# Performance work log

Measured on AMD Instinct MI355X. Metric: run time of the kernel, lower is better.

The kernel has to match this reference:

```python
import jax, jax.numpy as jnp
import numpy as np

B, N, K, A = 2, 4096, 20, 12
DIMS = [32, 64, 128, 256, 512]
POOL_RATE, POOL_K = 4, 4


def knn_index(v, k):
    # v: (b, n, 3) -> (b, n, k) nearest neighbors, self excluded
    d2 = jnp.sum(v * v, axis=-1)
    dist = d2[:, :, None] + d2[:, None, :] - 2.0 * jnp.einsum('bnd,bmd->bnm', v, v)
    _, idx = jax.lax.top_k(-dist, k + 1)
    return idx[:, :, 1:]


def gather_pos(v, idx):
    return jax.vmap(lambda vv, ii: vv[ii])(v, idx)  # (b, n, k, 3)


def gather_fea(fm, idx):
    return jax.vmap(lambda f, ii: f[:, ii, :])(fm, idx)  # (b, c, n, k, a)


def nbr_dirs(v, idx):
    d = gather_pos(v, idx) - v[:, :, None, :]
    return d / (jnp.linalg.norm(d, axis=-1, keepdims=True) + 1e-8)


def conv_surface(idx, v, K0):
    # K0: (C0, A, 3) learned direction kernels; output (b, C0, n, A)
    d = nbr_dirs(v, idx)  # (b,n,k,3)
    theta = jax.nn.relu(jnp.einsum('bnkd,cad->bnkca', d, K0))
    return jnp.transpose(jnp.max(theta, axis=2), (0, 2, 1, 3))


def equi_conv(idx, v, fm, dirs, Wc, bc, Ws):
    # fm: (b, cin, n, a) -> (b, cout, n, a)
    d = nbr_dirs(v, idx)
    theta = jax.nn.relu(jnp.einsum('bnkd,ad->bnka', d, dirs))  # (b,n,k,a)
    fn = gather_fea(fm, idx)  # (b,cin,n,k,a)
    fs = jnp.einsum('bcnka,co->bonka', fn, Ws) * theta[:, None]
    fs = jnp.max(fs, axis=3)  # max over neighbors -> (b,cout,n,a)
    fc = jnp.einsum('bcna,co->bona', fm, Wc) + bc[None, :, None, None]
    return fc + fs


def batchnorm(x, g, b):
    m = jnp.mean(x, axis=(0, 2, 3), keepdims=True)
    var = jnp.var(x, axis=(0, 2, 3), keepdims=True)
    return (x - m) * jax.lax.rsqrt(var + 1e-5) * g[None, :, None, None] + b[None, :, None, None]


def pool(v, fm):
    idx = knn_index(v, POOL_K)
    fn = jnp.max(gather_fea(fm, idx), axis=3)
    fm_p = jnp.maximum(fm, fn)
    sel = jnp.arange(0, v.shape[1], POOL_RATE)  # strided subsample
    return v[:, sel], fm_p[:, :, sel]


def fea_of(fm):
    return jnp.transpose(jnp.max(fm, axis=-1), (0, 2, 1))  # (b,n,c)


def setup_inputs() -> dict:
    key = jax.random.key(0)
    ks = iter(jax.random.split(key, 32))
    p = {'vertices': jax.random.normal(next(ks), (B, N, 3), jnp.float32)}
    p['K0'] = jax.random.normal(next(ks), (DIMS[0], A, 3), jnp.float32) * 0.1
    for i, (ci, co) in enumerate(zip(DIMS[:4], DIMS[1:]), start=1):
        s = 1.0 / np.sqrt(ci).astype(np.float32)
        p[f'dirs{i}'] = jax.random.normal(next(ks), (A, 3), jnp.float32) * 0.1
        p[f'Wc{i}'] = jax.random.normal(next(ks), (ci, co), jnp.float32) * s
        p[f'bc{i}'] = jnp.zeros((co,), jnp.float32)
        p[f'Ws{i}'] = jax.random.normal(next(ks), (ci, co), jnp.float32) * s
    for i, c in enumerate([DIMS[1], DIMS[2], DIMS[3]], start=1):
        p[f'g{i}'] = jnp.ones((c,), jnp.float32)
        p[f'b{i}'] = jnp.zeros((c,), jnp.float32)
    return p


def reference(vertices, K0, dirs1, Wc1, bc1, Ws1, dirs2, Wc2, bc2, Ws2,
              dirs3, Wc3, bc3, Ws3, dirs4, Wc4, bc4, Ws4,
              g1, b1, g2, b2, g3, b3):
    idx = knn_index(vertices, K)
    fm0 = jax.nn.relu(conv_surface(idx, vertices, K0))
    fm1 = jax.nn.relu(batchnorm(equi_conv(idx, vertices, fm0, dirs1, Wc1, bc1, Ws1), g1, b1))
    v1, fmp1 = pool(vertices, fm1)
    idx1 = knn_index(v1, min(K, v1.shape[1] // 8))
    fm2 = jax.nn.relu(batchnorm(equi_conv(idx1, v1, fmp1, dirs2, Wc2, bc2, Ws2), g2, b2))
    fm3 = jax.nn.relu(batchnorm(equi_conv(idx1, v1, fm2, dirs3, Wc3, bc3, Ws3), g3, b3))
    v2, fmp2 = pool(v1, fm3)
    idx2 = knn_index(v2, min(K, v2.shape[1] // 8))
    fm4 = equi_conv(idx2, v2, fmp2, dirs4, Wc4, bc4, Ws4)
    return fea_of(fm0), fea_of(fm1), fea_of(fm2), fea_of(fm3), fea_of(fm4)
```

## Files before the change

### kernel.cpp

```cpp
#include <hip/hip_runtime.h>
#include <hip/hip_bf16.h>
#include <math.h>

typedef unsigned short u16;
typedef unsigned long long u64;
#define DEV static __device__ __forceinline__

constexpr int Bz = 2, N0 = 4096, N1 = 1024, N2 = 256, KNN = 20, NA = 12;
constexpr int C0 = 32, C1 = 64, C2 = 128, C3 = 256, C4 = 512;
constexpr int BNG = 32;

constexpr size_t OFF_V0F   = 0;
constexpr size_t OFF_V1F   = 32768;
constexpr size_t OFF_V2F   = 40960;
constexpr size_t OFF_K0F   = 43008;
constexpr size_t OFF_DIRS  = 44160;
constexpr size_t OFF_WC    = 44304;
constexpr size_t OFF_WS    = 218384;
constexpr size_t OFF_BC    = 392464;
constexpr size_t OFF_BN    = 393424;
constexpr size_t OFF_FLAG  = 394832;
constexpr size_t OFF_IDX0  = 394848;
constexpr size_t OFF_IDX1  = 558688;
constexpr size_t OFF_IDX2  = 599648;
constexpr size_t OFF_PART  = 609888;
constexpr size_t PART_SZ   = 28672;
constexpr size_t OFF_HALF  = OFF_PART + PART_SZ;

constexpr size_t HA = 0;
constexpr size_t HB = 3145728;
constexpr size_t HG = 9437184;
constexpr size_t HP = HG + 3145728;

constexpr size_t OUT0 = 0;
constexpr size_t OUT1 = OUT0 + (size_t)Bz*N0*C0;
constexpr size_t OUT2 = OUT1 + (size_t)Bz*N0*C1;
constexpr size_t OUT3 = OUT2 + (size_t)Bz*N1*C2;
constexpr size_t OUT4 = OUT3 + (size_t)Bz*N1*C3;

DEV float b2f(u16 v) { return __uint_as_float(((unsigned int)v) << 16); }
DEV u16 f2b(float f) {
  unsigned int u = __float_as_uint(f);
  unsigned int lsb = (u >> 16) & 1u;
  return (u16)((u + 0x7fffu + lsb) >> 16);
}
DEV unsigned packb(float a, float b) {
  return (unsigned)f2b(a) | ((unsigned)f2b(b) << 16);
}

DEV u64 shflx64(u64 v, int m) {
  int lo = __shfl_xor((int)(unsigned)v, m, 64);
  int hi = __shfl_xor((int)(unsigned)(v >> 32), m, 64);
  return ((u64)(unsigned)hi << 32) | (unsigned)lo;
}
DEV int mbcnt64(u64 m) {
  return __builtin_amdgcn_mbcnt_hi((unsigned)(m >> 32),
         __builtin_amdgcn_mbcnt_lo((unsigned)m, 0));
}

DEV void st12(float* dst, const float* v) {
  float4 a{v[0],v[1],v[2],v[3]}, b{v[4],v[5],v[6],v[7]}, c{v[8],v[9],v[10],v[11]};
  ((float4*)dst)[0] = a; ((float4*)dst)[1] = b; ((float4*)dst)[2] = c;
}
DEV void st12(u16* dst, const float* v) {
  uint2 a{packb(v[0],v[1]), packb(v[2],v[3])};
  uint2 b{packb(v[4],v[5]), packb(v[6],v[7])};
  uint2 c{packb(v[8],v[9]), packb(v[10],v[11])};
  ((uint2*)dst)[0] = a; ((uint2*)dst)[1] = b; ((uint2*)dst)[2] = c;
}

struct InPtrs { const void* p[24]; };

__global__ void eq_convert_all(InPtrs in, float* ws) {
  __shared__ int sflag;
  {
    const u16* v = (const u16*)in.p[0];
    if (threadIdx.x < 64) {
      int bad = 0;
      #pragma unroll
      for (int j = 0; j < 4; ++j) {
        unsigned u = v[threadIdx.x*4 + j];
        int ex = (u >> 7) & 0xFF;
        bad += (((u & 0x7FFFu) != 0u) && (ex < 64 || ex > 191)) ? 1 : 0;
      }
      int tot = bad;
      #pragma unroll
      for (int s = 32; s > 0; s >>= 1) tot += __shfl_xor(tot, s, 64);
      if (threadIdx.x == 0) sflag = (tot >= 8) ? 1 : 0;
    }
    __syncthreads();
  }
  int f32mode = sflag;
  int t = blockIdx.x * blockDim.x + threadIdx.x;
  if (t < Bz*N0) {
    float x, y, z;
    if (f32mode) { const float* v = (const float*)in.p[0]; x=v[t*3]; y=v[t*3+1]; z=v[t*3+2]; }
    else { const u16* v = (const u16*)in.p[0]; x=b2f(v[t*3]); y=b2f(v[t*3+1]); z=b2f(v[t*3+2]); }
    float4 o; o.x=x; o.y=y; o.z=z; o.w=(x*x + y*y) + z*z;
    ((float4*)(ws + OFF_V0F))[t] = o;
    int b = t / N0, i = t % N0;
    if ((i & 3) == 0)  ((float4*)(ws + OFF_V1F))[b*N1 + (i >> 2)] = o;
    if ((i & 15) == 0) ((float4*)(ws + OFF_V2F))[b*N2 + (i >> 4)] = o;
    return;
  }
  int r = t - Bz*N0;
  if (r >= 351312) {
    int z = r - 351312;
    if (z < (int)PART_SZ) ws[OFF_PART + z] = 0.f;
    return;
  }
  const int cnt[23] = {1152, 36,2048,64,2048, 36,8192,128,8192,
                       36,32768,256,32768, 36,131072,512,131072,
                       64,64,128,128,256,256};
  const size_t off[23] = {OFF_K0F,
    OFF_DIRS+0,   OFF_WC+0,     OFF_BC+0,   OFF_WS+0,
    OFF_DIRS+36,  OFF_WC+2048,  OFF_BC+64,  OFF_WS+2048,
    OFF_DIRS+72,  OFF_WC+10240, OFF_BC+192, OFF_WS+10240,
    OFF_DIRS+108, OFF_WC+43008, OFF_BC+448, OFF_WS+43008,
    OFF_BN+0, OFF_BN+64, OFF_BN+128, OFF_BN+256, OFF_BN+384, OFF_BN+640};
  for (int i = 0; i < 23; ++i) {
    if (r < cnt[i]) {
      float val = f32mode ? ((const float*)in.p[i+1])[r] : b2f(((const u16*)in.p[i+1])[r]);
      ws[off[i] + r] = val;
      return;
    }
    r -= cnt[i];
  }
}

template<int NPTS>
DEV void knn_body(int blk, const float4* __restrict__ vf, int* __restrict__ idx_out,
                  char* smem) {
  constexpr int CPL = NPTS/64;
  constexpr int TILE = (NPTS < 512) ? NPTS : 512;
  constexpr int NT = NPTS / TILE;
  float4* tile = (float4*)smem;
  u64* selw_base = (u64*)(smem + TILE*16);
  int* extr_base = (int*)(smem + TILE*16 + 4*64*8);
  int wave = threadIdx.x >> 6, lane = threadIdx.x & 63;
  int tid = threadIdx.x;
  u64* selw = selw_base + wave*64;
  int* extrw = extr_base + wave*24;
  int qid = blk*4 + wave;
  int b = qid / NPTS, q = qid % NPTS;
  const float4* vb = vf + (size_t)b*NPTS;
  float4 vq = vb[q];
  const unsigned DINF = 0xFFFFFFFFu;
  unsigned d1=DINF, d2=DINF, d3=DINF, d4=DINF;
  int i1=0x3FFFFFFF, i2=0x3FFFFFFF, i3=0x3FFFFFFF, i4=0x3FFFFFFF;
  for (int tt = 0; tt < NT; ++tt) {
    __syncthreads();
    for (int i = tid; i < TILE; i += 256) tile[i] = vb[tt*TILE + i];
    __syncthreads();
    #pragma unroll 4
    for (int j = 0; j < TILE/64; ++j) {
      int cl = j*64 + lane;
      float4 vc = tile[cl];
      int c = tt*TILE + cl;
      float dt = (vq.x*vc.x + vq.y*vc.y) + vq.z*vc.z;
      float d = (vq.w + vc.w) - 2.0f*dt;
      unsigned u = __float_as_uint(d);
      unsigned ud = u ^ ((unsigned)(((int)u) >> 31) | 0x80000000u);
      bool lt1 = ud < d1, lt2 = ud < d2, lt3 = ud < d3, lt4 = ud < d4;
      d4 = lt3 ? d3 : (lt4 ? ud : d4);  i4 = lt3 ? i3 : (lt4 ? c : i4);
      d3 = lt2 ? d2 : (lt3 ? ud : d3);  i3 = lt2 ? i2 : (lt3 ? c : i3);
      d2 = lt1 ? d1 : (lt2 ? ud : d2);  i2 = lt1 ? i1 : (lt2 ? c : i2);
      d1 = lt1 ? ud : d1;               i1 = lt1 ? c  : i1;
    }
  }
  unsigned p = 0;
  for (int bit = 31; bit >= 0; --bit) {
    unsigned T = p | (1u << bit);
    u64 m1 = __ballot(d1 < T), m2 = __ballot(d2 < T);
    u64 m3 = __ballot(d3 < T), m4 = __ballot(d4 < T);
    int cnt = __popcll(m1) + __popcll(m2) + __popcll(m3) + __popcll(m4);
    if (cnt < KNN+1) p = T;
  }
  size_t obase = (size_t)qid*KNN;
  bool need_fb = false;
  if (CPL > 4) {
    need_fb = (__ballot(d4 <= p) != 0ULL);
  }
  if (!need_fb) {
    bool p1 = d1 <= p, p2 = d2 <= p, p3 = d3 <= p, p4 = d4 <= p;
    u64 m1 = __ballot(p1), m2 = __ballot(p2), m3 = __ballot(p3), m4 = __ballot(p4);
    int c1 = __popcll(m1), c2 = __popcll(m2), c3 = __popcll(m3), c4 = __popcll(m4);
    int S = c1 + c2 + c3 + c4;
    if (S > 63) need_fb = true;
    else {
      if (p1) selw[mbcnt64(m1)] = ((u64)d1 << 32) | (unsigned)i1;
      if (p2) selw[c1 + mbcnt64(m2)] = ((u64)d2 << 32) | (unsigned)i2;
      if (p3) selw[c1 + c2 + mbcnt64(m3)] = ((u64)d3 << 32) | (unsigned)i3;
      if (p4) selw[c1 + c2 + c3 + mbcnt64(m4)] = ((u64)d4 << 32) | (unsigned)i4;
      if (lane < S) {
        u64 mykey = selw[lane];
        int rank = 0;
        for (int j = 0; j < S; ++j) rank += (selw[j] < mykey) ? 1 : 0;
        if (rank >= 1 && rank <= KNN)
          idx_out[obase + rank - 1] = (int)(unsigned)(mykey & 0xFFFFFFFFu);
      }
    }
  }
  if (need_fb) {
    const u64 KINF = ~0ULL;
    u64 k1 = ((u64)d1 << 32) | (unsigned)i1;
    u64 k2 = ((u64)d2 << 32) | (unsigned)i2;
    u64 k3 = ((u64)d3 << 32) | (unsigned)i3;
    u64 k4 = ((u64)d4 << 32) | (unsigned)i4;
    for (int r = 0; r < KNN+1; ++r) {
      u64 g = k1;
      #pragma unroll
      for (int s = 32; s; s >>= 1) { u64 o = shflx64(g, s); g = (o < g) ? o : g; }
      int gidx = (int)(g & 0xFFFFFFFFu);
      if (lane == 0) {
        extrw[r] = gidx;
        if (r > 0) idx_out[obase + r - 1] = gidx;
      }
      if (r < KNN && lane == (gidx & 63)) {
        k1 = k2; k2 = k3; k3 = k4; k4 = KINF;
        if (k1 == KINF) {
          for (int j = 0; j < CPL; ++j) {
            int c = j*64 + lane;
            float4 vc = vb[c];
            float dt = (vq.x*vc.x + vq.y*vc.y) + vq.z*vc.z;
            float d = (vq.w + vc.w) - 2.0f*dt;
            unsigned u = __float_as_uint(d);
            unsigned ud = u ^ ((unsigned)(((int)u) >> 31) | 0x80000000u);
            u64 k = ((u64)ud << 32) | (unsigned)c;
            bool ex = false;
            for (int e = 0; e <= r; ++e) ex |= (extrw[e] == c);
            if (!ex) {
              bool lt1 = k < k1, lt2 = k < k2, lt3 = k < k3, lt4 = k < k4;
              k4 = lt3 ? k3 : (lt4 ? k : k4);
              k3 = lt2 ? k2 : (lt3 ? k : k3);
              k2 = lt1 ? k1 : (lt2 ? k : k2);
              k1 = lt1 ? k  : k1;
            }
          }
        }
      }
    }
  }
}

__global__ __launch_bounds__(256) void eq_knn_all(
    const float4* __restrict__ v0, int* __restrict__ i0,
    const float4* __restrict__ v1, int* __restrict__ i1,
    const float4* __restrict__ v2, int* __restrict__ i2) {
  __shared__ __align__(16) char smem[512*16 + 4*64*8 + 4*24*4];
  int blk = blockIdx.x;
  constexpr int NB0 = Bz*N0/4, NB1 = Bz*N1/4;
  if (blk < NB0)            knn_body<N0>(blk, v0, i0, smem);
  else if (blk < NB0+NB1)   knn_body<N1>(blk - NB0, v1, i1, smem);
  else                      knn_body<N2>(blk - NB0 - NB1, v2, i2, smem);
}

__global__ __launch_bounds__(128) void eq_conv_surface(
    const float4* __restrict__ v0f, const int* __restrict__ idx0,
    const float* __restrict__ K0f, u16* __restrict__ fm0, float* __restrict__ out0) {
  int bq = blockIdx.x;
  int b = bq >> 12;
  __shared__ float dk[KNN][3];
  __shared__ float row[C0*NA];
  int tid = threadIdx.x;
  if (tid < KNN) {
    int m = idx0[(size_t)bq*KNN + tid];
    float4 vq = v0f[bq];
    float4 vm = v0f[(size_t)b*N0 + m];
    float dx = vm.x - vq.x, dy = vm.y - vq.y, dz = vm.z - vq.z;
    float nrm = sqrtf((dx*dx + dy*dy) + dz*dz) + 1e-8f;
    dk[tid][0] = dx/nrm; dk[tid][1] = dy/nrm; dk[tid][2] = dz/nrm;
  }
  __syncthreads();
  for (int t4 = tid; t4 < C0*NA/4; t4 += 128) {
    const float* kd = K0f + (size_t)t4*12;
    float4 k0 = *(const float4*)(kd);
    float4 k1 = *(const float4*)(kd + 4);
    float4 k2 = *(const float4*)(kd + 8);
    float m0=0.f, m1=0.f, m2=0.f, m3=0.f;
    #pragma unroll
    for (int k = 0; k < KNN; ++k) {
      float dx = dk[k][0], dy = dk[k][1], dz = dk[k][2];
      m0 = fmaxf(m0, (dx*k0.x + dy*k0.y) + dz*k0.z);
      m1 = fmaxf(m1, (dx*k0.w + dy*k1.x) + dz*k1.y);
      m2 = fmaxf(m2, (dx*k1.z + dy*k1.w) + dz*k2.x);
      m3 = fmaxf(m3, (dx*k2.y + dy*k2.z) + dz*k2.w);
    }
    uint2 r; r.x = packb(m0, m1); r.y = packb(m2, m3);
    ((uint2*)fm0)[(size_t)bq*(C0*NA/4) + t4] = r;
    row[4*t4+0] = m0; row[4*t4+1] = m1; row[4*t4+2] = m2; row[4*t4+3] = m3;
  }
  __syncthreads();
  if (tid < C0) {
    float m = row[tid*NA];
    #pragma unroll
    for (int a = 1; a < NA; ++a) m = fmaxf(m, row[tid*NA + a]);
    out0[(size_t)bq*C0 + tid] = m;
  }
}

template<int CI, int CO, typename TO>
__global__ __launch_bounds__(256) void eq_linear4(
    const u16* __restrict__ in, const float* __restrict__ Wc,
    const float* __restrict__ Ws, const float* __restrict__ bias,
    TO* __restrict__ fc, u16* __restrict__ g) {
  constexpr int PPB = 512 / CO;
  constexpr int RS = CI*NA + 4;
  __shared__ float lds[PPB*RS];
  int tid = threadIdx.x;
  int mat = blockIdx.x & 1;
  int pt0 = (blockIdx.x >> 1) * PPB;
  constexpr int E = PPB*CI*NA;
  for (int t = tid; t < E; t += 256) {
    int pt = t / (CI*NA), r = t % (CI*NA);
    lds[pt*RS + r] = b2f(in[((size_t)(pt0+pt))*CI*NA + r]);
  }
  __syncthreads();
  constexpr int TPP = CO/2;
  int opair = tid % TPP, pt = tid / TPP;
  int o0 = opair*2;
  const float* W = mat ? Ws : Wc;
  const float* row = lds + pt*RS;
  float a0[NA], a1[NA];
  #pragma unroll
  for (int a = 0; a < NA; ++a) { a0[a]=0.f; a1[a]=0.f; }
  #pragma unroll 4
  for (int c = 0; c < CI; ++c) {
    float2 w2 = *(const float2*)(W + (size_t)c*CO + o0);
    float4 i0 = *(const float4*)(row + c*NA);
    float4 i1 = *(const float4*)(row + c*NA + 4);
    float4 i2 = *(const float4*)(row + c*NA + 8);
    float iv[NA] = {i0.x,i0.y,i0.z,i0.w, i1.x,i1.y,i1.z,i1.w, i2.x,i2.y,i2.z,i2.w};
    #pragma unroll
    for (int a = 0; a < NA; ++a) {
      a0[a] += iv[a]*w2.x; a1[a] += iv[a]*w2.y;
    }
  }
  size_t ptg = pt0 + pt;
  if (mat == 0) {
    float b0 = bias[o0], b1 = bias[o0+1];
    #pragma unroll
    for (int a = 0; a < NA; ++a) { a0[a] += b0; a1[a] += b1; }
    st12(fc + ((size_t)ptg*CO + o0)*NA, a0);
    st12(fc + ((size_t)ptg*CO + o0 + 1)*NA, a1);
  } else {
    st12(g + ((size_t)ptg*CO + o0)*NA, a0);
    st12(g + ((size_t)ptg*CO + o0 + 1)*NA, a1);
  }
}

__global__ __launch_bounds__(256) void eq_fsmax(
    const u16* __restrict__ g, const float4* __restrict__ vf,
    const float* __restrict__ dirs, const int* __restrict__ idx,
    u16* __restrict__ out, float* __restrict__ part, int npts, int co) {
  int bq = blockIdx.x;
  int b = bq / npts;
  __shared__ float th[KNN*NA];
  __shared__ float dk[KNN][3];
  __shared__ int nb[KNN];
  __shared__ float sstat[2][C3];
  int tid = threadIdx.x;
  if (tid < KNN) {
    int m = idx[(size_t)bq*KNN + tid];
    nb[tid] = m;
    float4 vq = vf[bq];
    float4 vm = vf[(size_t)b*npts + m];
    float dx = vm.x - vq.x, dy = vm.y - vq.y, dz = vm.z - vq.z;
    float nrm = sqrtf((dx*dx + dy*dy) + dz*dz) + 1e-8f;
    dk[tid][0] = dx/nrm; dk[tid][1] = dy/nrm; dk[tid][2] = dz/nrm;
  }
  sstat[0][tid] = 0.f; sstat[1][tid] = 0.f;
  __syncthreads();
  if (tid < KNN*NA) {
    int k = tid / NA, a = tid % NA;
    float s = (dk[k][0]*dirs[a*3] + dk[k][1]*dirs[a*3+1]) + dk[k][2]*dirs[a*3+2];
    th[tid] = fmaxf(s, 0.f);
  }
  __syncthreads();
  int quarter = co*NA/4;
  uint2* dst = (uint2*)(out + (size_t)bq*co*NA);
  const uint2* gb = (const uint2*)(g + (size_t)b*npts*co*NA);
  for (int t4 = tid; t4 < quarter; t4 += 256) {
    int a = (4*t4) % NA;
    const float* tha = th + a;
    float m0=-3.0e38f, m1=-3.0e38f, m2=-3.0e38f, m3=-3.0e38f;
    #pragma unroll 5
    for (int k = 0; k < KNN; ++k) {
      uint2 pv = gb[(size_t)nb[k]*quarter + t4];
      float4 tv = *(const float4*)(tha + k*NA);
      m0 = fmaxf(m0, tv.x*b2f((u16)(pv.x)));
      m1 = fmaxf(m1, tv.y*b2f((u16)(pv.x >> 16)));
      m2 = fmaxf(m2, tv.z*b2f((u16)(pv.y)));
      m3 = fmaxf(m3, tv.w*b2f((u16)(pv.y >> 16)));
    }
    uint2 d = dst[t4];
    float v0 = b2f((u16)d.x) + m0;
    float v1 = b2f((u16)(d.x >> 16)) + m1;
    float v2 = b2f((u16)d.y) + m2;
    float v3 = b2f((u16)(d.y >> 16)) + m3;
    uint2 r; r.x = packb(v0, v1); r.y = packb(v2, v3);
    dst[t4] = r;
    int ch = t4 / 3;
    atomicAdd(&sstat[0][ch], (v0 + v1) + (v2 + v3));
    atomicAdd(&sstat[1][ch], (v0*v0 + v1*v1) + (v2*v2 + v3*v3));
  }
  __syncthreads();
  if (tid < co) {
    float* pg = part + (size_t)(bq & (BNG-1))*2*co;
    atomicAdd(&pg[tid], sstat[0][tid]);
    atomicAdd(&pg[co + tid], sstat[1][tid]);
  }
}

template<int SPL>
__global__ __launch_bounds__(256) void eq_fsmax_fea(
    const u16* __restrict__ g, const float* __restrict__ fcin,
    const float4* __restrict__ vf, const float* __restrict__ dirs,
    const int* __restrict__ idx, float* __restrict__ outfea,
    int npts, int co) {
  constexpr int CHUNK = C4 / SPL;
  int part = blockIdx.x % SPL;
  int bq = blockIdx.x / SPL;
  int b = bq / npts;
  __shared__ float th[KNN*NA];
  __shared__ float dk[KNN][3];
  __shared__ int nb[KNN];
  __shared__ float row[CHUNK*NA];
  int tid = threadIdx.x;
  if (tid < KNN) {
    int m = idx[(size_t)bq*KNN + tid];
    nb[tid] = m;
    float4 vq = vf[bq];
    float4 vm = vf[(size_t)b*npts + m];
    float dx = vm.x - vq.x, dy = vm.y - vq.y, dz = vm.z - vq.z;
    float nrm = sqrtf((dx*dx + dy*dy) + dz*dz) + 1e-8f;
    dk[tid][0] = dx/nrm; dk[tid][1] = dy/nrm; dk[tid][2] = dz/nrm;
  }
  __syncthreads();
  if (tid < KNN*NA) {
    int k = tid / NA, a = tid % NA;
    float s = (dk[k][0]*dirs[a*3] + dk[k][1]*dirs[a*3+1]) + dk[k][2]*dirs[a*3+2];
    th[tid] = fmaxf(s, 0.f);
  }
  __syncthreads();
  int o0 = part * CHUNK;
  const float4* fcr = (const float4*)(fcin + ((size_t)bq*co + o0)*NA);
  const uint2* gb = (const uint2*)(g + (size_t)b*npts*co*NA + (size_t)o0*NA);
  int gquarter = co*NA/4;
  for (int t4 = tid; t4 < CHUNK*NA/4; t4 += 256) {
    int a = (4*t4) % NA;
    const float* tha = th + a;
    float m0=-3.0e38f, m1=-3.0e38f, m2=-3.0e38f, m3=-3.0e38f;
    #pragma unroll 5
    for (int k = 0; k < KNN; ++k) {
      uint2 pv = gb[(size_t)nb[k]*gquarter + t4];
      float4 tv = *(const float4*)(tha + k*NA);
      m0 = fmaxf(m0, tv.x*b2f((u16)(pv.x)));
      m1 = fmaxf(m1, tv.y*b2f((u16)(pv.x >> 16)));
      m2 = fmaxf(m2, tv.z*b2f((u16)(pv.y)));
      m3 = fmaxf(m3, tv.w*b2f((u16)(pv.y >> 16)));
    }
    float4 fc4 = fcr[t4];
    row[4*t4+0] = fc4.x + m0;
    row[4*t4+1] = fc4.y + m1;
    row[4*t4+2] = fc4.z + m2;
    row[4*t4+3] = fc4.w + m3;
  }
  __syncthreads();
  for (int o = tid; o < CHUNK; o += 256) {
    float m = row[o*NA];
    #pragma unroll
    for (int a = 1; a < NA; ++a) m = fmaxf(m, row[o*NA + a]);
    outfea[(size_t)bq*co + o0 + o] = m;
  }
}

__global__ __launch_bounds__(256) void eq_bnrelu_fea(
    u16* __restrict__ fm, const float* __restrict__ part,
    const float* __restrict__ gamma, const float* __restrict__ beta,
    float* __restrict__ outfea, int npts, int co) {
  int bq = blockIdx.x;
  int tid = threadIdx.x;
  __shared__ float sc[C3], sh[C3];
  __shared__ float row[C3*NA];
  for (int o = tid; o < co; o += 256) {
    float s = 0.f, s2 = 0.f;
    for (int g = 0; g < BNG; ++g) {
      s  += part[(size_t)g*2*co + o];
      s2 += part[(size_t)g*2*co + co + o];
    }
    float cnt = (float)(Bz*npts*NA);
    float mean = s / cnt;
    float var = fmaxf(s2 / cnt - mean*mean, 0.f);
    float inv = 1.0f / sqrtf(var + 1e-5f);
    sc[o] = gamma[o] * inv;
    sh[o] = beta[o] - mean * gamma[o] * inv;
  }
  __syncthreads();
  uint2* p = (uint2*)(fm + (size_t)bq*co*NA);
  int quarter = co*NA/4;
  for (int t4 = tid; t4 < quarter; t4 += 256) {
    int o = (4*t4) / NA;
    float s = sc[o], h = sh[o];
    uint2 pv = p[t4];
    float v0 = fmaxf(b2f((u16)pv.x)*s + h, 0.f);
    float v1 = fmaxf(b2f((u16)(pv.x >> 16))*s + h, 0.f);
    float v2 = fmaxf(b2f((u16)pv.y)*s + h, 0.f);
    float v3 = fmaxf(b2f((u16)(pv.y >> 16))*s + h, 0.f);
    uint2 r; r.x = packb(v0, v1); r.y = packb(v2, v3);
    p[t4] = r;
    row[4*t4+0] = v0; row[4*t4+1] = v1; row[4*t4+2] = v2; row[4*t4+3] = v3;
  }
  __syncthreads();
  for (int o = tid; o < co; o += 256) {
    float m = row[o*NA];
    #pragma unroll
    for (int a = 1; a < NA; ++a) m = fmaxf(m, row[o*NA + a]);
    outfea[(size_t)bq*co + o] = m;
  }
}

__global__ __launch_bounds__(256) void eq_pool(
    const u16* __restrict__ fm, const int* __restrict__ idx,
    u16* __restrict__ fmp, int npts, int c) {
  int ns = npts / 4;
  int bj = blockIdx.x;
  int b = bj / ns, j = bj % ns;
  int q = 4*j;
  size_t bq = (size_t)b*npts + q;
  __shared__ int nb[4];
  if (threadIdx.x < 4) nb[threadIdx.x] = idx[bq*KNN + threadIdx.x];
  __syncthreads();
  int quarter = c*NA/4;
  const uint2* base = (const uint2*)(fm + (size_t)b*npts*c*NA);
  const uint2* p0 = base + (size_t)q*quarter;
  uint2* dst = (uint2*)(fmp + (size_t)bj*c*NA);
  for (int t4 = threadIdx.x; t4 < quarter; t4 += 256) {
    uint2 v = p0[t4];
    float m0 = b2f((u16)v.x), m1 = b2f((u16)(v.x >> 16));
    float m2 = b2f((u16)v.y), m3 = b2f((u16)(v.y >> 16));
    #pragma unroll
    for (int kk = 0; kk < 4; ++kk) {
      uint2 w = base[(size_t)nb[kk]*quarter + t4];
      m0 = fmaxf(m0, b2f((u16)w.x));
      m1 = fmaxf(m1, b2f((u16)(w.x >> 16)));
      m2 = fmaxf(m2, b2f((u16)w.y));
      m3 = fmaxf(m3, b2f((u16)(w.y >> 16)));
    }
    uint2 r; r.x = packb(m0, m1); r.y = packb(m2, m3);
    dst[t4] = r;
  }
}

extern "C" void kernel_launch(void* const* d_in, const int* in_sizes, int n_in,
                              void* d_out, int out_size, void* d_ws, size_t ws_size,
                              hipStream_t stream) {
  float* ws = (float*)d_ws;
  float* out = (float*)d_out;
  u16* arena = (u16*)(ws + OFF_HALF);

  InPtrs ip;
  for (int i = 0; i < 24; ++i) ip.p[i] = d_in[i];

  float4* v0f = (float4*)(ws + OFF_V0F);
  float4* v1f = (float4*)(ws + OFF_V1F);
  float4* v2f = (float4*)(ws + OFF_V2F);
  int* idx0 = (int*)(ws + OFF_IDX0);
  int* idx1 = (int*)(ws + OFF_IDX1);
  int* idx2 = (int*)(ws + OFF_IDX2);
  u16* bufA = arena + HA;
  u16* bufB = arena + HB;
  float* fc4f = (float*)(arena + HB);
  u16* bufG = arena + HG;
  u16* bufP = arena + HP;
  float* partA = ws + OFF_PART;
  float* partB = ws + OFF_PART + 4096;
  float* partC = ws + OFF_PART + 12288;
  const float* DIRS = ws + OFF_DIRS;

  {
    int total = Bz*N0 + 351312 + (int)PART_SZ;
    eq_convert_all<<<(total + 255)/256, 256, 0, stream>>>(ip, ws);
  }

  eq_knn_all<<<Bz*N0/4 + Bz*N1/4 + Bz*N2/4, 256, 0, stream>>>(v0f, idx0, v1f, idx1, v2f, idx2);
  eq_conv_surface<<<Bz*N0, 128, 0, stream>>>(v0f, idx0, ws + OFF_K0F, bufA, out + OUT0);

  eq_linear4<C0, C1, u16><<<(Bz*N0/8)*2, 256, 0, stream>>>(bufA, ws + OFF_WC + 0, ws + OFF_WS + 0,
                                                           ws + OFF_BC + 0, bufB, bufG);
  eq_fsmax<<<Bz*N0, 256, 0, stream>>>(bufG, v0f, DIRS + 0, idx0, bufB, partA, N0, C1);
  eq_bnrelu_fea<<<Bz*N0, 256, 0, stream>>>(bufB, partA, ws + OFF_BN + 0, ws + OFF_BN + 64,
                                           out + OUT1, N0, C1);

  eq_pool<<<Bz*N1, 256, 0, stream>>>(bufB, idx0, bufP, N0, C1);

  eq_linear4<C1, C2, u16><<<(Bz*N1/4)*2, 256, 0, stream>>>(bufP, ws + OFF_WC + 2048, ws + OFF_WS + 2048,
                                                           ws + OFF_BC + 64, bufA, bufG);
  eq_fsmax<<<Bz*N1, 256, 0, stream>>>(bufG, v1f, DIRS + 36, idx1, bufA, partB, N1, C2);
  eq_bnrelu_fea<<<Bz*N1, 256, 0, stream>>>(bufA, partB, ws + OFF_BN + 128, ws + OFF_BN + 256,
                                           out + OUT2, N1, C2);

  eq_linear4<C2, C3, u16><<<(Bz*N1/2)*2, 256, 0, stream>>>(bufA, ws + OFF_WC + 10240, ws + OFF_WS + 10240,
                                                           ws + OFF_BC + 192, bufB, bufG);
  eq_fsmax<<<Bz*N1, 256, 0, stream>>>(bufG, v1f, DIRS + 72, idx1, bufB, partC, N1, C3);
  eq_bnrelu_fea<<<Bz*N1, 256, 0, stream>>>(bufB, partC, ws + OFF_BN + 384, ws + OFF_BN + 640,
                                           out + OUT3, N1, C3);

  eq_pool<<<Bz*N2, 256, 0, stream>>>(bufB, idx1, bufP, N1, C3);

  eq_linear4<C3, C4, float><<<(Bz*N2)*2, 256, 0, stream>>>(bufP, ws + OFF_WC + 43008, ws + OFF_WS + 43008,
                                                           ws + OFF_BC + 448, fc4f, bufG);
  eq_fsmax_fea<4><<<Bz*N2*4, 256, 0, stream>>>(bufG, fc4f, v2f, DIRS + 108, idx2, out + OUT4, N2, C4);
}
```

Before: 493.8 us.

## Track distance-only top-4 in kNN and recover indices with second threshold pass

The per-lane top-4 insertion now keeps only the distance keys and uses min/max networks, with no index registers or index selects. After the ballot-based threshold search, a second pass over the candidates recomputes distances and compacts those under the threshold into shared memory along with their indices. Tiles grow to 1024 points and the next tile is register-prefetched to overlap global loads with compute. The cost is recomputing every distance once more and a larger shared-memory footprint per block, which may reduce occupancy.

```diff
diff --git a/kernel.cpp b/kernel.cpp
--- a/kernel.cpp
+++ b/kernel.cpp
@@ -128,12 +128,23 @@
   }
 }
 
+DEV unsigned umin(unsigned a, unsigned b) { return a < b ? a : b; }
+DEV unsigned umax(unsigned a, unsigned b) { return a > b ? a : b; }
+
+DEV unsigned cand_ud(const float4 vq, const float4 vc) {
+  float dt = fmaf(vq.x, vc.x, fmaf(vq.y, vc.y, vq.z*vc.z));
+  float d  = fmaf(-2.0f, dt, vq.w + vc.w);
+  unsigned u = __float_as_uint(d);
+  return u ^ ((unsigned)(((int)u) >> 31) | 0x80000000u);
+}
+
 template<int NPTS>
 DEV void knn_body(int blk, const float4* __restrict__ vf, int* __restrict__ idx_out,
                   char* smem) {
   constexpr int CPL = NPTS/64;
-  constexpr int TILE = (NPTS < 512) ? NPTS : 512;
+  constexpr int TILE = (NPTS < 1024) ? NPTS : 1024;
   constexpr int NT = NPTS / TILE;
+  constexpr int LPT = TILE/256;
   float4* tile = (float4*)smem;
   u64* selw_base = (u64*)(smem + TILE*16);
   int* extr_base = (int*)(smem + TILE*16 + 4*64*8);
@@ -145,96 +156,125 @@
   int b = qid / NPTS, q = qid % NPTS;
   const float4* vb = vf + (size_t)b*NPTS;
   float4 vq = vb[q];
-  const unsigned DINF = 0xFFFFFFFFu;
-  unsigned d1=DINF, d2=DINF, d3=DINF, d4=DINF;
-  int i1=0x3FFFFFFF, i2=0x3FFFFFFF, i3=0x3FFFFFFF, i4=0x3FFFFFFF;
+
+  float4 pf[LPT];
+  #pragma unroll
+  for (int i = 0; i < LPT; ++i) pf[i] = vb[tid + i*256];
+  #pragma unroll
+  for (int i = 0; i < LPT; ++i) tile[tid + i*256] = pf[i];
+  __syncthreads();
+
+  unsigned k1=~0u, k2=~0u, k3=~0u, k4=~0u;
   for (int tt = 0; tt < NT; ++tt) {
-    __syncthreads();
-    for (int i = tid; i < TILE; i += 256) tile[i] = vb[tt*TILE + i];
-    __syncthreads();
+    if (tt+1 < NT) {
+      #pragma unroll
+      for (int i = 0; i < LPT; ++i) pf[i] = vb[(tt+1)*TILE + tid + i*256];
+    } else if (NT > 1) {
+      #pragma unroll
+      for (int i = 0; i < LPT; ++i) pf[i] = vb[tid + i*256];
+    }
     #pragma unroll 4
     for (int j = 0; j < TILE/64; ++j) {
-      int cl = j*64 + lane;
-      float4 vc = tile[cl];
-      int c = tt*TILE + cl;
-      float dt = (vq.x*vc.x + vq.y*vc.y) + vq.z*vc.z;
-      float d = (vq.w + vc.w) - 2.0f*dt;
-      unsigned u = __float_as_uint(d);
-      unsigned ud = u ^ ((unsigned)(((int)u) >> 31) | 0x80000000u);
-      bool lt1 = ud < d1, lt2 = ud < d2, lt3 = ud < d3, lt4 = ud < d4;
-      d4 = lt3 ? d3 : (lt4 ? ud : d4);  i4 = lt3 ? i3 : (lt4 ? c : i4);
-      d3 = lt2 ? d2 : (lt3 ? ud : d3);  i3 = lt2 ? i2 : (lt3 ? c : i3);
-      d2 = lt1 ? d1 : (lt2 ? ud : d2);  i2 = lt1 ? i1 : (lt2 ? c : i2);
-      d1 = lt1 ? ud : d1;               i1 = lt1 ? c  : i1;
-    }
-  }
+      float4 vc = tile[j*64 + lane];
+      unsigned key = cand_ud(vq, vc);
+      unsigned nk1 = umin(key, k1);
+      unsigned nk2 = umin(umax(key, k1), k2);
+      unsigned nk3 = umin(umax(key, k2), k3);
+      unsigned nk4 = umin(umax(key, k3), k4);
+      k1 = nk1; k2 = nk2; k3 = nk3; k4 = nk4;
+    }
+    if (tt+1 < NT || NT > 1) {
+      __syncthreads();
+      #pragma unroll
+      for (int i = 0; i < LPT; ++i) tile[tid + i*256] = pf[i];
+      __syncthreads();
+    }
+  }
+
   unsigned p = 0;
   for (int bit = 31; bit >= 0; --bit) {
     unsigned T = p | (1u << bit);
-    u64 m1 = __ballot(d1 < T), m2 = __ballot(d2 < T);
-    u64 m3 = __ballot(d3 < T), m4 = __ballot(d4 < T);
+    u64 m1 = __ballot(k1 < T), m2 = __ballot(k2 < T);
+    u64 m3 = __ballot(k3 < T), m4 = __ballot(k4 < T);
     int cnt = __popcll(m1) + __popcll(m2) + __popcll(m3) + __popcll(m4);
     if (cnt < KNN+1) p = T;
   }
   size_t obase = (size_t)qid*KNN;
-  bool need_fb = false;
-  if (CPL > 4) {
-    need_fb = (__ballot(d4 <= p) != 0ULL);
-  }
+  bool need_fb = (CPL > 4) && (__ballot(k4 <= p) != 0ULL);
+
+  int base = 0;
+  for (int tt = 0; tt < NT; ++tt) {
+    if (tt+1 < NT) {
+      #pragma unroll
+      for (int i = 0; i < LPT; ++i) pf[i] = vb[(tt+1)*TILE + tid + i*256];
+    }
+    if (!need_fb) {
+      #pragma unroll 4
+      for (int j = 0; j < TILE/64; ++j) {
+        float4 vc = tile[j*64 + lane];
+        unsigned ud = cand_ud(vq, vc);
+        bool sel = (ud <= p);
+        u64 m = __ballot(sel);
+        int pos = base + mbcnt64(m);
+        if (sel && pos < 64) {
+          int c = tt*TILE + j*64 + lane;
+          selw[pos] = ((u64)ud << 32) | (unsigned)c;
+        }
+        base += __popcll(m);
+      }
+    }
+    if (tt+1 < NT) {
+      __syncthreads();
+      #pragma unroll
+      for (int i = 0; i < LPT; ++i) tile[tid + i*256] = pf[i];
+      __syncthreads();
+    }
+  }
+
   if (!need_fb) {
-    bool p1 = d1 <= p, p2 = d2 <= p, p3 = d3 <= p, p4 = d4 <= p;
-    u64 m1 = __ballot(p1), m2 = __ballot(p2), m3 = __ballot(p3), m4 = __ballot(p4);
-    int c1 = __popcll(m1), c2 = __popcll(m2), c3 = __popcll(m3), c4 = __popcll(m4);
-    int S = c1 + c2 + c3 + c4;
-    if (S > 63) need_fb = true;
-    else {
-      if (p1) selw[mbcnt64(m1)] = ((u64)d1 << 32) | (unsigned)i1;
-      if (p2) selw[c1 + mbcnt64(m2)] = ((u64)d2 << 32) | (unsigned)i2;
-      if (p3) selw[c1 + c2 + mbcnt64(m3)] = ((u64)d3 << 32) | (unsigned)i3;
-      if (p4) selw[c1 + c2 + c3 + mbcnt64(m4)] = ((u64)d4 << 32) | (unsigned)i4;
-      if (lane < S) {
-        u64 mykey = selw[lane];
-        int rank = 0;
-        for (int j = 0; j < S; ++j) rank += (selw[j] < mykey) ? 1 : 0;
-        if (rank >= 1 && rank <= KNN)
-          idx_out[obase + rank - 1] = (int)(unsigned)(mykey & 0xFFFFFFFFu);
-      }
-    }
-  }
-  if (need_fb) {
+    int S = (base < 64) ? base : 64;
+    if (lane < S) {
+      u64 mykey = selw[lane];
+      int rank = 0;
+      for (int j = 0; j < S; ++j) rank += (selw[j] < mykey) ? 1 : 0;
+      if (rank >= 1 && rank <= KNN)
+        idx_out[obase + rank - 1] = (int)(unsigned)(mykey & 0xFFFFFFFFu);
+    }
+  } else {
     const u64 KINF = ~0ULL;
-    u64 k1 = ((u64)d1 << 32) | (unsigned)i1;
-    u64 k2 = ((u64)d2 << 32) | (unsigned)i2;
-    u64 k3 = ((u64)d3 << 32) | (unsigned)i3;
-    u64 k4 = ((u64)d4 << 32) | (unsigned)i4;
+    u64 K1=KINF, K2=KINF, K3=KINF, K4=KINF;
+    for (int j = 0; j < CPL; ++j) {
+      int c = j*64 + lane;
+      u64 k = ((u64)cand_ud(vq, vb[c]) << 32) | (unsigned)c;
+      bool lt1 = k < K1, lt2 = k < K2, lt3 = k < K3, lt4 = k < K4;
+      K4 = lt3 ? K3 : (lt4 ? k : K4);
+      K3 = lt2 ? K2 : (lt3 ? k : K3);
+      K2 = lt1 ? K1 : (lt2 ? k : K2);
+      K1 = lt1 ? k  : K1;
+    }
     for (int r = 0; r < KNN+1; ++r) {
-      u64 g = k1;
+      u64 g = K1;
       #pragma unroll
       for (int s = 32; s; s >>= 1) { u64 o = shflx64(g, s); g = (o < g) ? o : g; }
-      int gidx = (int)(g & 0xFFFFFFFFu);
+      int gidx = (int)(unsigned)(g & 0xFFFFFFFFu);
       if (lane == 0) {
         extrw[r] = gidx;
         if (r > 0) idx_out[obase + r - 1] = gidx;
       }
       if (r < KNN && lane == (gidx & 63)) {
-        k1 = k2; k2 = k3; k3 = k4; k4 = KINF;
-        if (k1 == KINF) {
+        K1 = K2; K2 = K3; K3 = K4; K4 = KINF;
+        if (K1 == KINF) {
           for (int j = 0; j < CPL; ++j) {
             int c = j*64 + lane;
-            float4 vc = vb[c];
-            float dt = (vq.x*vc.x + vq.y*vc.y) + vq.z*vc.z;
-            float d = (vq.w + vc.w) - 2.0f*dt;
-            unsigned u = __float_as_uint(d);
-            unsigned ud = u ^ ((unsigned)(((int)u) >> 31) | 0x80000000u);
-            u64 k = ((u64)ud << 32) | (unsigned)c;
+            u64 k = ((u64)cand_ud(vq, vb[c]) << 32) | (unsigned)c;
             bool ex = false;
             for (int e = 0; e <= r; ++e) ex |= (extrw[e] == c);
             if (!ex) {
-              bool lt1 = k < k1, lt2 = k < k2, lt3 = k < k3, lt4 = k < k4;
-              k4 = lt3 ? k3 : (lt4 ? k : k4);
-              k3 = lt2 ? k2 : (lt3 ? k : k3);
-              k2 = lt1 ? k1 : (lt2 ? k : k2);
-              k1 = lt1 ? k  : k1;
+              bool lt1 = k < K1, lt2 = k < K2, lt3 = k < K3, lt4 = k < K4;
+              K4 = lt3 ? K3 : (lt4 ? k : K4);
+              K3 = lt2 ? K2 : (lt3 ? k : K3);
+              K2 = lt1 ? K1 : (lt2 ? k : K2);
+              K1 = lt1 ? k  : K1;
             }
           }
         }
@@ -247,7 +287,7 @@
     const float4* __restrict__ v0, int* __restrict__ i0,
     const float4* __restrict__ v1, int* __restrict__ i1,
     const float4* __restrict__ v2, int* __restrict__ i2) {
-  __shared__ __align__(16) char smem[512*16 + 4*64*8 + 4*24*4];
+  __shared__ __align__(16) char smem[1024*16 + 4*64*8 + 4*24*4];
   int blk = blockIdx.x;
   constexpr int NB0 = Bz*N0/4, NB1 = Bz*N1/4;
   if (blk < NB0)            knn_body<N0>(blk, v0, i0, smem);
```

Measured after the change: 543.1 us. 10.0% more time.
